# Kernel tuning notes

Hardware: AMD Instinct MI355X
Metric: run time of the kernel (lower is better)

Reference implementation:

```python
import jax, jax.numpy as jnp
import numpy as np

B, C, H, W = 16, 64, 64, 64
HW = H * W            # = dim = 4096
R = 4                 # reduction_ratio
NH = 8                # head_num
EPS = 1e-5


def setup_inputs() -> dict:
    key = jax.random.key(0)
    ks = jax.random.split(key, 8)
    s = 0.02  # weight init scale
    return {
        "x": jax.random.normal(ks[0], (B, C, H, W), jnp.float32),
        "ln1_w": jnp.ones((C,), jnp.float32),
        "ln1_b": jnp.zeros((C,), jnp.float32),
        "ln2_w": jnp.ones((C,), jnp.float32),
        "ln2_b": jnp.zeros((C,), jnp.float32),
        "W_rk": jax.random.normal(ks[1], (C * R, C), jnp.float32) * s,
        "W_rv": jax.random.normal(ks[2], (C * R, C), jnp.float32) * s,
        "W_q": jax.random.normal(ks[3], (HW, HW), jnp.float32) * s,
        "W_k": jax.random.normal(ks[4], (HW // R, HW // R), jnp.float32) * s,
        "W_v": jax.random.normal(ks[5], (HW // R, HW // R), jnp.float32) * s,
        "W_o": jax.random.normal(ks[6], (HW, HW), jnp.float32) * s,
    }


def _ln(x, w, b):
    # LayerNorm over last axis
    mu = jnp.mean(x, axis=-1, keepdims=True)
    var = jnp.mean((x - mu) ** 2, axis=-1, keepdims=True)
    return (x - mu) / jnp.sqrt(var + EPS) * w + b


def reference(x, ln1_w, ln1_b, ln2_w, ln2_b, W_rk, W_rv, W_q, W_k, W_v, W_o):
    b, c, h, w = x.shape
    hw = h * w
    # ln1: LayerNorm2d == per-pixel LayerNorm over channels
    xn = _ln(x.transpose(0, 2, 3, 1), ln1_w, ln1_b)      # [B,H,W,C]
    xf = xn.reshape(b, hw, c)                            # [B,HW,C] (row-major HW)
    # K/V spatial reduction: 'a (cd r) b -> a cd (b r)'
    kv = xf.reshape(b, hw // R, R, c).transpose(0, 1, 3, 2).reshape(b, hw // R, c * R)
    k = _ln(kv @ W_rk, ln2_w, ln2_b)                     # [B,HW/R,C]
    v = _ln(kv @ W_rv, ln2_w, ln2_b)                     # [B,HW/R,C]
    # projections over the SPATIAL axis (dim = HW)
    q = xf.transpose(0, 2, 1) @ W_q                      # [B,C,HW]
    k = k.transpose(0, 2, 1) @ W_k                       # [B,C,HW/R]
    v = v.transpose(0, 2, 1) @ W_v                       # [B,C,HW/R]
    Lq = hw // NH
    Lk = (hw // R) // NH
    # split heads along spatial axis, attend over channel dim C
    qh = q.reshape(b, c, NH, Lq).transpose(0, 2, 3, 1)   # [B,h,Lq,C]
    kh = k.reshape(b, c, NH, Lk).transpose(0, 2, 3, 1)   # [B,h,Lk,C]
    vh = v.reshape(b, c, NH, Lk).transpose(0, 2, 3, 1)   # [B,h,Lk,C]
    scale = float(hw // NH) ** 0.5
    attn = jax.nn.softmax(jnp.einsum('bhqc,bhkc->bhqk', qh, kh) / scale, axis=-1)
    # dropout is identity at inference
    o = jnp.einsum('bhqk,bhkc->bhqc', attn, vh)          # [B,h,Lq,C]
    # concat_head: heads become outer blocks of the spatial axis
    o = o.transpose(0, 3, 1, 2).reshape(b, c, hw)        # [B,C,HW]
    o = o @ W_o                                          # [B,C,HW]
    return o.reshape(b, c, h, w) + x
```

## Files before the change

### kernel.cpp

```cpp
#include <hip/hip_runtime.h>

typedef unsigned short u16;
typedef unsigned int u32;
typedef __attribute__((ext_vector_type(8))) __bf16 bf16x8;
typedef __attribute__((ext_vector_type(4))) float f32x4;
typedef __attribute__((ext_vector_type(4))) unsigned int u32x4;

#define MFMA16(a, b, c) __builtin_amdgcn_mfma_f32_16x16x32_bf16((a), (b), (c), 0, 0, 0)

__device__ __forceinline__ u16 f2bf(float f) {
  unsigned u = __float_as_uint(f);
  u += 0x7FFFu + ((u >> 16) & 1u);
  return (u16)(u >> 16);
}

typedef __attribute__((address_space(1))) const unsigned char gU8;
typedef __attribute__((address_space(3))) unsigned char sU8;
__device__ __forceinline__ void gload16(const void* g, void* l) {
  __builtin_amdgcn_global_load_lds((gU8*)g, (sU8*)l, 16, 0, 0);
}

__device__ __forceinline__ void wt_body(const float* __restrict__ W, u16* __restrict__ Wt,
                                        int K, int N, int bid, float* tile) {
  int ntn = N >> 6;
  int kt = bid / ntn, nt = bid % ntn;
  int t = threadIdx.x;
  const float* src = W + (size_t)kt * 64 * N + (size_t)nt * 64;
  f32x4 r[4];
#pragma unroll
  for (int i = 0; i < 4; ++i) {
    int idx = t + i * 256, row = idx >> 4, c4 = idx & 15;
    r[i] = *(const f32x4*)&src[(size_t)row * N + c4 * 4];
  }
#pragma unroll
  for (int i = 0; i < 4; ++i) {
    int idx = t + i * 256, row = idx >> 4, c4 = idx & 15;
#pragma unroll
    for (int j = 0; j < 4; ++j) tile[row * 65 + c4 * 4 + j] = r[i][j];
  }
  __syncthreads();
  int nn0 = t >> 3, k8 = t & 7;
  float v[2][8];
#pragma unroll
  for (int i = 0; i < 2; ++i)
#pragma unroll
    for (int j = 0; j < 8; ++j) v[i][j] = tile[(k8 * 8 + j) * 65 + nn0 + i * 32];
  u16* dst = Wt + (size_t)nt * 64 * K + (size_t)kt * 64;
#pragma unroll
  for (int i = 0; i < 2; ++i) {
    u32x4 pk;
#pragma unroll
    for (int j = 0; j < 4; ++j)
      pk[j] = (u32)f2bf(v[i][2 * j]) | ((u32)f2bf(v[i][2 * j + 1]) << 16);
    *(u32x4*)&dst[(size_t)(nn0 + i * 32) * K + k8 * 8] = pk;
  }
}

__device__ __forceinline__ void wperm_body(const float* __restrict__ Wrk, const float* __restrict__ Wrv,
                                           u16* __restrict__ Wtk, u16* __restrict__ Wtv, int bid) {
  int idx = bid * 256 + threadIdx.x;
  int cp = idx >> 8, f = idx & 255;
  int k = ((f & 63) << 2) | (f >> 6);
  Wtk[idx] = f2bf(Wrk[k * 64 + cp]);
  Wtv[idx] = f2bf(Wrv[k * 64 + cp]);
}

__device__ __forceinline__ void ln1_body(const float* __restrict__ x, const float* __restrict__ w,
                                         const float* __restrict__ bias, u16* __restrict__ xf_pc,
                                         u16* __restrict__ xfT, int bid, float* tile) {
  int b = bid >> 6, p0 = (bid & 63) << 6;
  int t = threadIdx.x;
  const float* xb = x + (size_t)b * 64 * 4096;
  f32x4 r[4];
#pragma unroll
  for (int i = 0; i < 4; ++i) {
    int idx = t + i * 256, c = idx >> 4, p4 = idx & 15;
    r[i] = *(const f32x4*)&xb[(size_t)c * 4096 + p0 + p4 * 4];
  }
#pragma unroll
  for (int i = 0; i < 4; ++i) {
    int idx = t + i * 256, c = idx >> 4, p4 = idx & 15;
#pragma unroll
    for (int j = 0; j < 4; ++j) tile[c * 65 + p4 * 4 + j] = r[i][j];
  }
  __syncthreads();
  int lane = t & 63, wvx = t >> 6;
  float gw = w[lane], gb = bias[lane];
#pragma unroll
  for (int pp = 0; pp < 16; pp += 2) {
    int p = wvx * 16 + pp;
    float v0 = tile[lane * 65 + p], v1 = tile[lane * 65 + p + 1];
    float s0 = v0, q0 = v0 * v0, s1 = v1, q1 = v1 * v1;
#pragma unroll
    for (int m = 1; m < 64; m <<= 1) {
      s0 += __shfl_xor(s0, m); q0 += __shfl_xor(q0, m);
      s1 += __shfl_xor(s1, m); q1 += __shfl_xor(q1, m);
    }
    float mu0 = s0 * (1.0f / 64.0f), var0 = q0 * (1.0f / 64.0f) - mu0 * mu0;
    float mu1 = s1 * (1.0f / 64.0f), var1 = q1 * (1.0f / 64.0f) - mu1 * mu1;
    tile[lane * 65 + p]     = (v0 - mu0) * rsqrtf(var0 + 1e-5f) * gw + gb;
    tile[lane * 65 + p + 1] = (v1 - mu1) * rsqrtf(var1 + 1e-5f) * gw + gb;
  }
  __syncthreads();
  u16* xfb = xf_pc + (size_t)b * 4096 * 64;
  u16* xtb = xfT + (size_t)b * 64 * 4096;
  int i0 = t >> 3, j8 = t & 7;
  float vc[2][8];
#pragma unroll
  for (int i = 0; i < 2; ++i)
#pragma unroll
    for (int j = 0; j < 8; ++j) vc[i][j] = tile[(j8 * 8 + j) * 65 + i0 + i * 32];
#pragma unroll
  for (int i = 0; i < 2; ++i) {
    u32x4 pk;
#pragma unroll
    for (int j = 0; j < 4; ++j)
      pk[j] = (u32)f2bf(vc[i][2 * j]) | ((u32)f2bf(vc[i][2 * j + 1]) << 16);
    *(u32x4*)&xfb[(size_t)(p0 + i0 + i * 32) * 64 + j8 * 8] = pk;
  }
  float vr[2][8];
#pragma unroll
  for (int i = 0; i < 2; ++i)
#pragma unroll
    for (int j = 0; j < 8; ++j) vr[i][j] = tile[(i0 + i * 32) * 65 + j8 * 8 + j];
#pragma unroll
  for (int i = 0; i < 2; ++i) {
    u32x4 pk;
#pragma unroll
    for (int j = 0; j < 4; ++j)
      pk[j] = (u32)f2bf(vr[i][2 * j]) | ((u32)f2bf(vr[i][2 * j + 1]) << 16);
    *(u32x4*)&xtb[(size_t)(i0 + i * 32) * 4096 + p0 + j8 * 8] = pk;
  }
}

__global__ __launch_bounds__(256) void prep_kernel(
    const float* __restrict__ W_q, u16* __restrict__ Wt_q,
    const float* __restrict__ W_o, u16* __restrict__ Wt_o,
    const float* __restrict__ W_k, u16* __restrict__ Wt_k,
    const float* __restrict__ W_v, u16* __restrict__ Wt_v,
    const float* __restrict__ W_rk, const float* __restrict__ W_rv,
    u16* __restrict__ Wt_rk, u16* __restrict__ Wt_rv,
    const float* __restrict__ x, const float* __restrict__ ln1w, const float* __restrict__ ln1b,
    u16* __restrict__ xf_pc, u16* __restrict__ xfT) {
  __shared__ float tile[64 * 65];
  int bid = blockIdx.x;
  if (bid < 4096)       wt_body(W_q, Wt_q, 4096, 4096, bid, tile);
  else if (bid < 8192)  wt_body(W_o, Wt_o, 4096, 4096, bid - 4096, tile);
  else if (bid < 8448)  wt_body(W_k, Wt_k, 1024, 1024, bid - 8192, tile);
  else if (bid < 8704)  wt_body(W_v, Wt_v, 1024, 1024, bid - 8448, tile);
  else if (bid < 8768)  wperm_body(W_rk, W_rv, Wt_rk, Wt_rv, bid - 8704);
  else                  ln1_body(x, ln1w, ln1b, xf_pc, xfT, bid - 8768, tile);
}

__global__ __launch_bounds__(256) void kv_kernel(const u16* __restrict__ xf_pc,
                                                 const u16* __restrict__ Wtk, const u16* __restrict__ Wtv,
                                                 const float* __restrict__ ln2w, const float* __restrict__ ln2b,
                                                 u16* __restrict__ kT, u16* __restrict__ vT) {
  __shared__ __align__(16) u16 As[64 * 264];
  __shared__ __align__(16) u16 Bk[64 * 264];
  __shared__ __align__(16) u16 Bv[64 * 264];
  u16* Tk = As;
  u16* Tv = As + 64 * 72;
  int b = blockIdx.x >> 4, s0 = (blockIdx.x & 15) << 6;
  int t = threadIdx.x;
  const u16* Asrc = xf_pc + (size_t)b * 4096 * 64 + (size_t)s0 * 256;
#pragma unroll
  for (int i = 0; i < 8; ++i) {
    int id = t + i * 256, row = id >> 5, c16 = id & 31;
    *(u32x4*)&As[row * 264 + c16 * 8] = *(const u32x4*)&Asrc[(size_t)row * 256 + c16 * 8];
    *(u32x4*)&Bk[row * 264 + c16 * 8] = *(const u32x4*)&Wtk[(size_t)row * 256 + c16 * 8];
    *(u32x4*)&Bv[row * 264 + c16 * 8] = *(const u32x4*)&Wtv[(size_t)row * 256 + c16 * 8];
  }
  __syncthreads();
  int lane = t & 63, wv = t >> 6, lo = lane & 15, hi = lane >> 4;
  f32x4 acck[4] = {}, accv[4] = {};
  int arow = (wv * 16 + lo) * 264 + hi * 8;
#pragma unroll
  for (int kk = 0; kk < 8; ++kk) {
    bf16x8 a = *(const bf16x8*)&As[arow + kk * 32];
#pragma unroll
    for (int nf = 0; nf < 4; ++nf) {
      bf16x8 bk = *(const bf16x8*)&Bk[(nf * 16 + lo) * 264 + kk * 32 + hi * 8];
      bf16x8 bv = *(const bf16x8*)&Bv[(nf * 16 + lo) * 264 + kk * 32 + hi * 8];
      acck[nf] = MFMA16(a, bk, acck[nf]);
      accv[nf] = MFMA16(a, bv, accv[nf]);
    }
  }
  __syncthreads();
  float w2[4], b2[4];
#pragma unroll
  for (int nf = 0; nf < 4; ++nf) { w2[nf] = ln2w[nf * 16 + lo]; b2[nf] = ln2b[nf * 16 + lo]; }
#pragma unroll
  for (int r = 0; r < 4; ++r) {
    float sk = 0.f, sk2 = 0.f, sv = 0.f, sv2 = 0.f;
#pragma unroll
    for (int nf = 0; nf < 4; ++nf) {
      float a = acck[nf][r], c = accv[nf][r];
      sk += a; sk2 += a * a; sv += c; sv2 += c * c;
    }
#pragma unroll
    for (int m = 1; m < 16; m <<= 1) {
      sk += __shfl_xor(sk, m); sk2 += __shfl_xor(sk2, m);
      sv += __shfl_xor(sv, m); sv2 += __shfl_xor(sv2, m);
    }
    float mk = sk * (1.f / 64.f), vk = sk2 * (1.f / 64.f) - mk * mk, rk = rsqrtf(vk + 1e-5f);
    float mv = sv * (1.f / 64.f), vv = sv2 * (1.f / 64.f) - mv * mv, rv = rsqrtf(vv + 1e-5f);
    int srow = wv * 16 + hi * 4 + r;
#pragma unroll
    for (int nf = 0; nf < 4; ++nf) {
      Tk[(nf * 16 + lo) * 72 + srow] = f2bf((acck[nf][r] - mk) * rk * w2[nf] + b2[nf]);
      Tv[(nf * 16 + lo) * 72 + srow] = f2bf((accv[nf][r] - mv) * rv * w2[nf] + b2[nf]);
    }
  }
  __syncthreads();
  u16* kdst = kT + (size_t)b * 64 * 1024 + s0;
  u16* vdst = vT + (size_t)b * 64 * 1024 + s0;
#pragma unroll
  for (int i = 0; i < 16; ++i) {
    int idx = t + i * 256, cp = idx >> 6, s = idx & 63;
    kdst[(size_t)cp * 1024 + s] = Tk[cp * 72 + s];
    vdst[(size_t)cp * 1024 + s] = Tv[cp * 72 + s];
  }
}

__device__ __forceinline__ void stage32(const u16* Ab, const u16* Bb, int K, int kt,
                                        u16* As, u16* Bs, int wv, int lane) {
#pragma unroll
  for (int i = 0; i < 2; ++i) {
    int cb = wv * 2 + i;
    int c = cb * 64 + lane;
    int row = c >> 2, s = c & 3;
    int scol = (s ^ (row & 3)) << 3;
    gload16(Ab + (size_t)row * K + kt * 32 + scol, As + cb * 512);
    gload16(Bb + (size_t)row * K + kt * 32 + scol, Bs + cb * 512);
  }
}

__device__ __forceinline__ void compute32(const u16* As, const u16* Bs, f32x4 acc[4][4],
                                          int wm, int wn, int lo, int hi) {
  int slot = (hi ^ (lo & 3)) << 3;
  bf16x8 a[4], bb[4];
#pragma unroll
  for (int i = 0; i < 4; ++i) {
    a[i]  = *(const bf16x8*)&As[(wm + i * 16 + lo) * 32 + slot];
    bb[i] = *(const bf16x8*)&Bs[(wn + i * 16 + lo) * 32 + slot];
  }
#pragma unroll
  for (int mi = 0; mi < 4; ++mi)
#pragma unroll
    for (int ni = 0; ni < 4; ++ni)
      acc[mi][ni] = MFMA16(a[mi], bb[ni], acc[mi][ni]);
}

template <int EPI>
__device__ void gemm_body(const u16* __restrict__ A, const u16* __restrict__ Bm,
                          u16* __restrict__ Cc, int N, int K, int chunkStride,
                          int mt, int nt, int koff, int nk, u16* lds) {
  int t = threadIdx.x, lane = t & 63, wv = t >> 6;
  int wm = (wv >> 1) * 64, wn = (wv & 1) * 64;
  int lo = lane & 15, hi = lane >> 4;
  f32x4 acc[4][4] = {};
  const u16* Ab = A + (size_t)mt * 128 * K + koff;
  const u16* Bb = Bm + (size_t)nt * 128 * K + koff;
  u16* bufs[3] = {lds, lds + 8192, lds + 16384};
  stage32(Ab, Bb, K, 0, bufs[0], bufs[0] + 4096, wv, lane);
  stage32(Ab, Bb, K, 1, bufs[1], bufs[1] + 4096, wv, lane);
  for (int kt = 0; kt < nk; ++kt) {
    if (kt + 1 < nk) asm volatile("s_waitcnt vmcnt(4)" ::: "memory");
    else             asm volatile("s_waitcnt vmcnt(0)" ::: "memory");
    __builtin_amdgcn_s_barrier();
    __builtin_amdgcn_sched_barrier(0);
    if (kt + 2 < nk) {
      u16* nb = bufs[(kt + 2) % 3];
      stage32(Ab, Bb, K, kt + 2, nb, nb + 4096, wv, lane);
    }
    u16* cb = bufs[kt % 3];
    compute32(cb, cb + 4096, acc, wm, wn, lo, hi);
  }
#pragma unroll
  for (int mi = 0; mi < 4; ++mi)
#pragma unroll
    for (int ni = 0; ni < 4; ++ni)
#pragma unroll
      for (int r = 0; r < 4; ++r) {
        int m = mt * 128 + wm + mi * 16 + hi * 4 + r;
        int n = nt * 128 + wn + ni * 16 + lo;
        float v = acc[mi][ni][r];
        if constexpr (EPI == 0) {
          Cc[(size_t)m * N + n] = f2bf(v);
        } else {
          Cc[(size_t)(n >> 6) * chunkStride + (size_t)m * 64 + (n & 63)] = f2bf(v);
        }
      }
}

__global__ __launch_bounds__(256, 3) void qkv_kernel(
    const u16* __restrict__ Wt_q, const u16* __restrict__ xfT, u16* __restrict__ q_t,
    const u16* __restrict__ Wt_k, const u16* __restrict__ k_lnT, u16* __restrict__ kproj,
    const u16* __restrict__ v_lnT, const u16* __restrict__ Wt_v, u16* __restrict__ vproj) {
  __shared__ __align__(16) u16 lds[24576];
  int bid = blockIdx.x;
  if (bid < 1024) {
    int log = (bid & 7) * 128 + (bid >> 3);
    int kh = log >> 8, tile = log & 255, mt = tile >> 3, nt = tile & 7;
    gemm_body<1>(Wt_q, xfT, q_t + (size_t)kh * 4194304, 1024, 4096, 4096 * 64,
                 mt, nt, kh * 1024, 32, lds);
  } else if (bid < 1088) {
    int id = bid - 1024;
    gemm_body<1>(Wt_k, k_lnT, kproj, 1024, 1024, 1024 * 64, id >> 3, id & 7, 0, 32, lds);
  } else {
    int id = bid - 1088;
    gemm_body<0>(v_lnT, Wt_v, vproj, 1024, 1024, 0, id >> 3, id & 7, 0, 32, lds);
  }
}

__global__ __launch_bounds__(256, 3) void ogemm_kernel(const u16* __restrict__ o2,
                                                       const u16* __restrict__ Wt_o,
                                                       u16* __restrict__ o_part) {
  __shared__ __align__(16) u16 lds[24576];
  int bid = blockIdx.x;
  int log = (bid & 7) * 64 + (bid >> 3);
  int kh = log >> 8, tile = log & 255, mt = tile >> 5, nt = tile & 31;
  gemm_body<0>(o2, Wt_o, o_part + (size_t)kh * 4194304, 4096, 4096, 0,
               mt, nt, kh * 2048, 64, lds);
}

__global__ __launch_bounds__(256) void oreduce_kernel(const float* __restrict__ x,
                                                      const u16* __restrict__ p0,
                                                      const u16* __restrict__ p1,
                                                      float* __restrict__ out) {
  size_t base = ((size_t)blockIdx.x * 256 + threadIdx.x) * 8;
  u32x4 a = *(const u32x4*)&p0[base];
  u32x4 b = *(const u32x4*)&p1[base];
  f32x4 x0 = *(const f32x4*)&x[base];
  f32x4 x1 = *(const f32x4*)&x[base + 4];
  float r[8];
#pragma unroll
  for (int j = 0; j < 4; ++j) {
    r[2 * j]     = __uint_as_float(a[j] << 16) + __uint_as_float(b[j] << 16);
    r[2 * j + 1] = __uint_as_float(a[j] & 0xFFFF0000u) + __uint_as_float(b[j] & 0xFFFF0000u);
  }
  f32x4 o0, o1;
#pragma unroll
  for (int j = 0; j < 4; ++j) { o0[j] = r[j] + x0[j]; o1[j] = r[4 + j] + x1[j]; }
  *(f32x4*)&out[base] = o0;
  *(f32x4*)&out[base + 4] = o1;
}

__global__ __launch_bounds__(256) void attn_kernel(const u16* __restrict__ qp, const u16* __restrict__ kp,
                                                   const u16* __restrict__ vp, u16* __restrict__ o2) {
  __shared__ __align__(16) u16 Qs[128 * 72];
  __shared__ __align__(16) u16 Ks[128 * 72];
  __shared__ __align__(16) u16 Vs[64 * 136];
  __shared__ __align__(16) u16 Ps[128 * 136];
  int qt = blockIdx.x & 3, h = (blockIdx.x >> 2) & 7, b = blockIdx.x >> 5;
  int t = threadIdx.x, lane = t & 63, wv = t >> 6;
  int lo = lane & 15, hi = lane >> 4;
  const u16* qsrc = qp + (size_t)b * 262144 + (size_t)(h * 512 + qt * 128) * 64;
  const u16* ksrc = kp + (size_t)b * 1024 * 64 + (size_t)(h * 128) * 64;
  const u16* vsrc = vp + (size_t)b * 64 * 1024 + h * 128;
#pragma unroll
  for (int i = 0; i < 4; ++i) {
    int id = t + i * 256, row = id >> 3, c8 = id & 7;
    size_t goff = (size_t)row * 64 + c8 * 8;
    float f[8] = {0.f, 0.f, 0.f, 0.f, 0.f, 0.f, 0.f, 0.f};
#pragma unroll
    for (int kh = 0; kh < 4; ++kh) {
      u32x4 pk = *(const u32x4*)&qsrc[(size_t)kh * 4194304 + goff];
#pragma unroll
      for (int j = 0; j < 4; ++j) {
        f[2 * j]     += __uint_as_float(pk[j] << 16);
        f[2 * j + 1] += __uint_as_float(pk[j] & 0xFFFF0000u);
      }
    }
    u32x4 pko;
#pragma unroll
    for (int j = 0; j < 4; ++j) pko[j] = (u32)f2bf(f[2 * j]) | ((u32)f2bf(f[2 * j + 1]) << 16);
    *(u32x4*)&Qs[row * 72 + c8 * 8] = pko;
  }
#pragma unroll
  for (int i = 0; i < 4; ++i) {
    int id = t + i * 256;
    int row = id >> 3, c16 = id & 7;
    *(u32x4*)&Ks[row * 72 + c16 * 8] = *(const u32x4*)&ksrc[(size_t)row * 64 + c16 * 8];
    int vrow = id >> 4, v16 = id & 15;
    *(u32x4*)&Vs[vrow * 136 + v16 * 8] = *(const u32x4*)&vsrc[(size_t)vrow * 1024 + v16 * 8];
  }
  __syncthreads();
  f32x4 s[2][8] = {};
#pragma unroll
  for (int kk = 0; kk < 2; ++kk) {
    bf16x8 a0 = *(const bf16x8*)&Qs[(wv * 32 + lo) * 72 + kk * 32 + hi * 8];
    bf16x8 a1 = *(const bf16x8*)&Qs[(wv * 32 + 16 + lo) * 72 + kk * 32 + hi * 8];
#pragma unroll
    for (int ni = 0; ni < 8; ++ni) {
      bf16x8 bb = *(const bf16x8*)&Ks[(ni * 16 + lo) * 72 + kk * 32 + hi * 8];
      s[0][ni] = MFMA16(a0, bb, s[0][ni]);
      s[1][ni] = MFMA16(a1, bb, s[1][ni]);
    }
  }
  const float inv_scale = 0.044194173824159216f;
#pragma unroll
  for (int mi = 0; mi < 2; ++mi)
#pragma unroll
    for (int ni = 0; ni < 8; ++ni) s[mi][ni] *= inv_scale;
#pragma unroll
  for (int mi = 0; mi < 2; ++mi) {
#pragma unroll
    for (int r = 0; r < 4; ++r) {
      float mx = -1e30f;
#pragma unroll
      for (int ni = 0; ni < 8; ++ni) mx = fmaxf(mx, s[mi][ni][r]);
#pragma unroll
      for (int m = 1; m < 16; m <<= 1) mx = fmaxf(mx, __shfl_xor(mx, m));
      float p[8], sum = 0.f;
#pragma unroll
      for (int ni = 0; ni < 8; ++ni) { p[ni] = __expf(s[mi][ni][r] - mx); sum += p[ni]; }
#pragma unroll
      for (int m = 1; m < 16; m <<= 1) sum += __shfl_xor(sum, m);
      float rs = 1.0f / sum;
      int row = wv * 32 + mi * 16 + hi * 4 + r;
#pragma unroll
      for (int ni = 0; ni < 8; ++ni) Ps[row * 136 + ni * 16 + lo] = f2bf(p[ni] * rs);
    }
  }
  __syncthreads();
  f32x4 o[4][2] = {};
#pragma unroll
  for (int kk = 0; kk < 4; ++kk) {
    bf16x8 b0 = *(const bf16x8*)&Ps[(wv * 32 + lo) * 136 + kk * 32 + hi * 8];
    bf16x8 b1 = *(const bf16x8*)&Ps[(wv * 32 + 16 + lo) * 136 + kk * 32 + hi * 8];
#pragma unroll
    for (int mi = 0; mi < 4; ++mi) {
      bf16x8 a = *(const bf16x8*)&Vs[(mi * 16 + lo) * 136 + kk * 32 + hi * 8];
      o[mi][0] = MFMA16(a, b0, o[mi][0]);
      o[mi][1] = MFMA16(a, b1, o[mi][1]);
    }
  }
  u16* od = o2 + (size_t)b * 64 * 4096 + h * 512 + qt * 128;
#pragma unroll
  for (int mi = 0; mi < 4; ++mi)
#pragma unroll
    for (int ni = 0; ni < 2; ++ni)
#pragma unroll
      for (int r = 0; r < 4; ++r) {
        int c = mi * 16 + hi * 4 + r;
        int lq = wv * 32 + ni * 16 + lo;
        od[(size_t)c * 4096 + lq] = f2bf(o[mi][ni][r]);
      }
}

extern "C" void kernel_launch(void* const* d_in, const int* in_sizes, int n_in,
                              void* d_out, int out_size, void* d_ws, size_t ws_size,
                              hipStream_t stream) {
  (void)in_sizes; (void)n_in; (void)out_size; (void)ws_size;
  const float* x    = (const float*)d_in[0];
  const float* ln1w = (const float*)d_in[1];
  const float* ln1b = (const float*)d_in[2];
  const float* ln2w = (const float*)d_in[3];
  const float* ln2b = (const float*)d_in[4];
  const float* W_rk = (const float*)d_in[5];
  const float* W_rv = (const float*)d_in[6];
  const float* W_q  = (const float*)d_in[7];
  const float* W_k  = (const float*)d_in[8];
  const float* W_v  = (const float*)d_in[9];
  const float* W_o  = (const float*)d_in[10];

  char* ws = (char*)d_ws;
  size_t off = 0;
  auto alloc = [&](size_t bytes) { char* p = ws + off; off += bytes; return p; };
  u16* Wt_q  = (u16*)alloc(4096ull * 4096 * 2);
  u16* Wt_o  = (u16*)alloc(4096ull * 4096 * 2);
  u16* Wt_k  = (u16*)alloc(1024ull * 1024 * 2);
  u16* Wt_v  = (u16*)alloc(1024ull * 1024 * 2);
  u16* Wt_rk = (u16*)alloc(64ull * 256 * 2);
  u16* Wt_rv = (u16*)alloc(64ull * 256 * 2);
  u16* xf_pc = (u16*)alloc(16ull * 4096 * 64 * 2);
  u16* xfT   = (u16*)alloc(16ull * 64 * 4096 * 2);
  u16* k_lnT = (u16*)alloc(16ull * 64 * 1024 * 2);
  u16* v_lnT = (u16*)alloc(16ull * 64 * 1024 * 2);
  u16* q_t   = (u16*)alloc(4ull * 16 * 4096 * 64 * 2);
  u16* kproj = (u16*)alloc(16ull * 1024 * 64 * 2);
  u16* vproj = (u16*)alloc(16ull * 64 * 1024 * 2);
  u16* o2     = xfT;
  u16* o_part = Wt_q;

  prep_kernel<<<9792, 256, 0, stream>>>(W_q, Wt_q, W_o, Wt_o, W_k, Wt_k, W_v, Wt_v,
                                        W_rk, W_rv, Wt_rk, Wt_rv, x, ln1w, ln1b, xf_pc, xfT);
  kv_kernel<<<256, 256, 0, stream>>>(xf_pc, Wt_rk, Wt_rv, ln2w, ln2b, k_lnT, v_lnT);
  qkv_kernel<<<1152, 256, 0, stream>>>(Wt_q, xfT, q_t, Wt_k, k_lnT, kproj, v_lnT, Wt_v, vproj);
  attn_kernel<<<512, 256, 0, stream>>>(q_t, kproj, vproj, o2);
  ogemm_kernel<<<512, 256, 0, stream>>>(o2, Wt_o, o_part);
  oreduce_kernel<<<2048, 256, 0, stream>>>(x, o_part, o_part + 4194304, (float*)d_out);
}
```

Measured before the change: 212.9 us.

## Fuse fp32 weight transpose and bf16 conversion into GEMM staging

Drops the separate prep pass that transposed W_q, W_o, W_k and W_v into bf16 workspace copies. The GEMMs now load fp32 weight tiles straight into registers, convert them to bf16 and write them into swizzled LDS, while the activation operand still uses async global-to-LDS loads. This removes a large read/write round trip of the weight matrices, at the cost of more global bytes per GEMM (fp32 instead of bf16), extra register pressure, and conversion work inside the pipelined main loop.

Measured after the change: 329.3 us. 54.7% more time.

```diff
diff --git a/kernel.cpp b/kernel.cpp
--- a/kernel.cpp
+++ b/kernel.cpp
@@ -18,42 +18,6 @@
 typedef __attribute__((address_space(3))) unsigned char sU8;
 __device__ __forceinline__ void gload16(const void* g, void* l) {
   __builtin_amdgcn_global_load_lds((gU8*)g, (sU8*)l, 16, 0, 0);
-}
-
-__device__ __forceinline__ void wt_body(const float* __restrict__ W, u16* __restrict__ Wt,
-                                        int K, int N, int bid, float* tile) {
-  int ntn = N >> 6;
-  int kt = bid / ntn, nt = bid % ntn;
-  int t = threadIdx.x;
-  const float* src = W + (size_t)kt * 64 * N + (size_t)nt * 64;
-  f32x4 r[4];
-#pragma unroll
-  for (int i = 0; i < 4; ++i) {
-    int idx = t + i * 256, row = idx >> 4, c4 = idx & 15;
-    r[i] = *(const f32x4*)&src[(size_t)row * N + c4 * 4];
-  }
-#pragma unroll
-  for (int i = 0; i < 4; ++i) {
-    int idx = t + i * 256, row = idx >> 4, c4 = idx & 15;
-#pragma unroll
-    for (int j = 0; j < 4; ++j) tile[row * 65 + c4 * 4 + j] = r[i][j];
-  }
-  __syncthreads();
-  int nn0 = t >> 3, k8 = t & 7;
-  float v[2][8];
-#pragma unroll
-  for (int i = 0; i < 2; ++i)
-#pragma unroll
-    for (int j = 0; j < 8; ++j) v[i][j] = tile[(k8 * 8 + j) * 65 + nn0 + i * 32];
-  u16* dst = Wt + (size_t)nt * 64 * K + (size_t)kt * 64;
-#pragma unroll
-  for (int i = 0; i < 2; ++i) {
-    u32x4 pk;
-#pragma unroll
-    for (int j = 0; j < 4; ++j)
-      pk[j] = (u32)f2bf(v[i][2 * j]) | ((u32)f2bf(v[i][2 * j + 1]) << 16);
-    *(u32x4*)&dst[(size_t)(nn0 + i * 32) * K + k8 * 8] = pk;
-  }
 }
 
 __device__ __forceinline__ void wperm_body(const float* __restrict__ Wrk, const float* __restrict__ Wrv,
@@ -134,22 +98,14 @@
 }
 
 __global__ __launch_bounds__(256) void prep_kernel(
-    const float* __restrict__ W_q, u16* __restrict__ Wt_q,
-    const float* __restrict__ W_o, u16* __restrict__ Wt_o,
-    const float* __restrict__ W_k, u16* __restrict__ Wt_k,
-    const float* __restrict__ W_v, u16* __restrict__ Wt_v,
     const float* __restrict__ W_rk, const float* __restrict__ W_rv,
     u16* __restrict__ Wt_rk, u16* __restrict__ Wt_rv,
     const float* __restrict__ x, const float* __restrict__ ln1w, const float* __restrict__ ln1b,
     u16* __restrict__ xf_pc, u16* __restrict__ xfT) {
   __shared__ float tile[64 * 65];
   int bid = blockIdx.x;
-  if (bid < 4096)       wt_body(W_q, Wt_q, 4096, 4096, bid, tile);
-  else if (bid < 8192)  wt_body(W_o, Wt_o, 4096, 4096, bid - 4096, tile);
-  else if (bid < 8448)  wt_body(W_k, Wt_k, 1024, 1024, bid - 8192, tile);
-  else if (bid < 8704)  wt_body(W_v, Wt_v, 1024, 1024, bid - 8448, tile);
-  else if (bid < 8768)  wperm_body(W_rk, W_rv, Wt_rk, Wt_rv, bid - 8704);
-  else                  ln1_body(x, ln1w, ln1b, xf_pc, xfT, bid - 8768, tile);
+  if (bid < 64) wperm_body(W_rk, W_rv, Wt_rk, Wt_rv, bid);
+  else          ln1_body(x, ln1w, ln1b, xf_pc, xfT, bid - 64, tile);
 }
 
 __global__ __launch_bounds__(256) void kv_kernel(const u16* __restrict__ xf_pc,
@@ -223,22 +179,46 @@
   }
 }
 
-__device__ __forceinline__ void stage32(const u16* Ab, const u16* Bb, int K, int kt,
-                                        u16* As, u16* Bs, int wv, int lane) {
+
+__device__ __forceinline__ void wload(const float* __restrict__ Wsrc, int Nw, int kbase, int wbase,
+                                      int t, f32x4 rr[4]) {
+  int r = t >> 4, j0 = (t & 15) * 4;
+  const float* p0 = Wsrc + (size_t)(kbase + 2 * r) * Nw + wbase + j0;
+  rr[0] = *(const f32x4*)p0;
+  rr[1] = *(const f32x4*)(p0 + Nw);
+  rr[2] = *(const f32x4*)(p0 + 64);
+  rr[3] = *(const f32x4*)(p0 + Nw + 64);
+}
+
+__device__ __forceinline__ void wstore(const f32x4 rr[4], int t, u16* As) {
+  int r = t >> 4, j0 = (t & 15) * 4;
+  int o = (2 * r) & 7;
+  int c = r >> 2;
+#pragma unroll
+  for (int i = 0; i < 2; ++i)
+#pragma unroll
+    for (int jj = 0; jj < 4; ++jj) {
+      int j = j0 + i * 64 + jj;
+      int s = c ^ ((j >> 2) & 3);
+      u32 pk = (u32)f2bf(rr[2 * i][jj]) | ((u32)f2bf(rr[2 * i + 1][jj]) << 16);
+      *(u32*)&As[j * 32 + s * 8 + o] = pk;
+    }
+}
+
+__device__ __forceinline__ void stageG(const u16* Gb, int K, int kt, u16* Bs, int wv, int lane) {
 #pragma unroll
   for (int i = 0; i < 2; ++i) {
     int cb = wv * 2 + i;
     int c = cb * 64 + lane;
     int row = c >> 2, s = c & 3;
-    int scol = (s ^ (row & 3)) << 3;
-    gload16(Ab + (size_t)row * K + kt * 32 + scol, As + cb * 512);
-    gload16(Bb + (size_t)row * K + kt * 32 + scol, Bs + cb * 512);
+    int scol = (s ^ ((row >> 2) & 3)) << 3;
+    gload16(Gb + (size_t)row * K + kt * 32 + scol, Bs + cb * 512);
   }
 }
 
 __device__ __forceinline__ void compute32(const u16* As, const u16* Bs, f32x4 acc[4][4],
                                           int wm, int wn, int lo, int hi) {
-  int slot = (hi ^ (lo & 3)) << 3;
+  int slot = (hi ^ ((lo >> 2) & 3)) << 3;
   bf16x8 a[4], bb[4];
 #pragma unroll
   for (int i = 0; i < 4; ++i) {
@@ -252,30 +232,64 @@
       acc[mi][ni] = MFMA16(a[mi], bb[ni], acc[mi][ni]);
 }
 
-template <int EPI>
-__device__ void gemm_body(const u16* __restrict__ A, const u16* __restrict__ Bm,
-                          u16* __restrict__ Cc, int N, int K, int chunkStride,
-                          int mt, int nt, int koff, int nk, u16* lds) {
+template <int EPI, int SIDE>
+__device__ void gemm_bodyW(const float* __restrict__ Wsrc, int Nw,
+                           const u16* __restrict__ Gm,
+                           u16* __restrict__ Cc, int N, int K, int chunkStride,
+                           int mt, int nt, int koff, int nk, u16* lds) {
   int t = threadIdx.x, lane = t & 63, wv = t >> 6;
   int wm = (wv >> 1) * 64, wn = (wv & 1) * 64;
   int lo = lane & 15, hi = lane >> 4;
   f32x4 acc[4][4] = {};
-  const u16* Ab = A + (size_t)mt * 128 * K + koff;
-  const u16* Bb = Bm + (size_t)nt * 128 * K + koff;
-  u16* bufs[3] = {lds, lds + 8192, lds + 16384};
-  stage32(Ab, Bb, K, 0, bufs[0], bufs[0] + 4096, wv, lane);
-  stage32(Ab, Bb, K, 1, bufs[1], bufs[1] + 4096, wv, lane);
-  for (int kt = 0; kt < nk; ++kt) {
-    if (kt + 1 < nk) asm volatile("s_waitcnt vmcnt(4)" ::: "memory");
-    else             asm volatile("s_waitcnt vmcnt(0)" ::: "memory");
+  int wbase = (SIDE == 0 ? mt : nt) * 128;
+  const u16* Gb = Gm + (size_t)(SIDE == 0 ? nt : mt) * 128 * K + koff;
+  u16* SW[3]; u16* SG[3];
+#pragma unroll
+  for (int b = 0; b < 3; ++b) {
+    u16* base = lds + b * 8192;
+    SW[b] = base;
+    SG[b] = base + 4096;
+  }
+  f32x4 rA[4], rB[4];
+  wload(Wsrc, Nw, koff, wbase, t, rA);
+  stageG(Gb, K, 0, SG[0], wv, lane);
+  wload(Wsrc, Nw, koff + 32, wbase, t, rB);
+  stageG(Gb, K, 1, SG[1], wv, lane);
+  wstore(rA, t, SW[0]);
+  for (int kt = 0; kt < nk; kt += 2) {
+    asm volatile("s_waitcnt vmcnt(2)" ::: "memory");
+    wstore(rB, t, SW[(kt + 1) % 3]);
+    asm volatile("s_waitcnt lgkmcnt(0)" ::: "memory");
     __builtin_amdgcn_s_barrier();
     __builtin_amdgcn_sched_barrier(0);
     if (kt + 2 < nk) {
-      u16* nb = bufs[(kt + 2) % 3];
-      stage32(Ab, Bb, K, kt + 2, nb, nb + 4096, wv, lane);
-    }
-    u16* cb = bufs[kt % 3];
-    compute32(cb, cb + 4096, acc, wm, wn, lo, hi);
+      wload(Wsrc, Nw, koff + (kt + 2) * 32, wbase, t, rA);
+      stageG(Gb, K, kt + 2, SG[(kt + 2) % 3], wv, lane);
+    }
+    {
+      u16* A_ = SIDE == 0 ? SW[kt % 3] : SG[kt % 3];
+      u16* B_ = SIDE == 0 ? SG[kt % 3] : SW[kt % 3];
+      compute32(A_, B_, acc, wm, wn, lo, hi);
+    }
+    int k1 = kt + 1;
+    if (k1 + 1 < nk) {
+      asm volatile("s_waitcnt vmcnt(2)" ::: "memory");
+      wstore(rA, t, SW[(k1 + 1) % 3]);
+    } else {
+      asm volatile("s_waitcnt vmcnt(0)" ::: "memory");
+    }
+    asm volatile("s_waitcnt lgkmcnt(0)" ::: "memory");
+    __builtin_amdgcn_s_barrier();
+    __builtin_amdgcn_sched_barrier(0);
+    if (k1 + 2 < nk) {
+      wload(Wsrc, Nw, koff + (k1 + 2) * 32, wbase, t, rB);
+      stageG(Gb, K, k1 + 2, SG[(k1 + 2) % 3], wv, lane);
+    }
+    {
+      u16* A_ = SIDE == 0 ? SW[k1 % 3] : SG[k1 % 3];
+      u16* B_ = SIDE == 0 ? SG[k1 % 3] : SW[k1 % 3];
+      compute32(A_, B_, acc, wm, wn, lo, hi);
+    }
   }
 #pragma unroll
   for (int mi = 0; mi < 4; ++mi)
@@ -295,34 +309,34 @@
 }
 
 __global__ __launch_bounds__(256, 3) void qkv_kernel(
-    const u16* __restrict__ Wt_q, const u16* __restrict__ xfT, u16* __restrict__ q_t,
-    const u16* __restrict__ Wt_k, const u16* __restrict__ k_lnT, u16* __restrict__ kproj,
-    const u16* __restrict__ v_lnT, const u16* __restrict__ Wt_v, u16* __restrict__ vproj) {
+    const float* __restrict__ W_q, const u16* __restrict__ xfT, u16* __restrict__ q_t,
+    const float* __restrict__ W_k, const u16* __restrict__ k_lnT, u16* __restrict__ kproj,
+    const u16* __restrict__ v_lnT, const float* __restrict__ W_v, u16* __restrict__ vproj) {
   __shared__ __align__(16) u16 lds[24576];
   int bid = blockIdx.x;
   if (bid < 1024) {
     int log = (bid & 7) * 128 + (bid >> 3);
     int kh = log >> 8, tile = log & 255, mt = tile >> 3, nt = tile & 7;
-    gemm_body<1>(Wt_q, xfT, q_t + (size_t)kh * 4194304, 1024, 4096, 4096 * 64,
-                 mt, nt, kh * 1024, 32, lds);
+    gemm_bodyW<1, 0>(W_q, 4096, xfT, q_t + (size_t)kh * 4194304, 1024, 4096, 4096 * 64,
+                     mt, nt, kh * 1024, 32, lds);
   } else if (bid < 1088) {
     int id = bid - 1024;
-    gemm_body<1>(Wt_k, k_lnT, kproj, 1024, 1024, 1024 * 64, id >> 3, id & 7, 0, 32, lds);
+    gemm_bodyW<1, 0>(W_k, 1024, k_lnT, kproj, 1024, 1024, 1024 * 64, id >> 3, id & 7, 0, 32, lds);
   } else {
     int id = bid - 1088;
-    gemm_body<0>(v_lnT, Wt_v, vproj, 1024, 1024, 0, id >> 3, id & 7, 0, 32, lds);
+    gemm_bodyW<0, 1>(W_v, 1024, v_lnT, vproj, 1024, 1024, 0, id >> 3, id & 7, 0, 32, lds);
   }
 }
 
 __global__ __launch_bounds__(256, 3) void ogemm_kernel(const u16* __restrict__ o2,
-                                                       const u16* __restrict__ Wt_o,
+                                                       const float* __restrict__ W_o,
                                                        u16* __restrict__ o_part) {
   __shared__ __align__(16) u16 lds[24576];
   int bid = blockIdx.x;
   int log = (bid & 7) * 64 + (bid >> 3);
   int kh = log >> 8, tile = log & 255, mt = tile >> 5, nt = tile & 31;
-  gemm_body<0>(o2, Wt_o, o_part + (size_t)kh * 4194304, 4096, 4096, 0,
-               mt, nt, kh * 2048, 64, lds);
+  gemm_bodyW<0, 1>(W_o, 4096, o2, o_part + (size_t)kh * 4194304, 4096, 4096, 0,
+                   mt, nt, kh * 2048, 64, lds);
 }
 
 __global__ __launch_bounds__(256) void oreduce_kernel(const float* __restrict__ x,
@@ -469,27 +483,22 @@
   char* ws = (char*)d_ws;
   size_t off = 0;
   auto alloc = [&](size_t bytes) { char* p = ws + off; off += bytes; return p; };
-  u16* Wt_q  = (u16*)alloc(4096ull * 4096 * 2);
-  u16* Wt_o  = (u16*)alloc(4096ull * 4096 * 2);
-  u16* Wt_k  = (u16*)alloc(1024ull * 1024 * 2);
-  u16* Wt_v  = (u16*)alloc(1024ull * 1024 * 2);
-  u16* Wt_rk = (u16*)alloc(64ull * 256 * 2);
-  u16* Wt_rv = (u16*)alloc(64ull * 256 * 2);
-  u16* xf_pc = (u16*)alloc(16ull * 4096 * 64 * 2);
-  u16* xfT   = (u16*)alloc(16ull * 64 * 4096 * 2);
-  u16* k_lnT = (u16*)alloc(16ull * 64 * 1024 * 2);
-  u16* v_lnT = (u16*)alloc(16ull * 64 * 1024 * 2);
-  u16* q_t   = (u16*)alloc(4ull * 16 * 4096 * 64 * 2);
-  u16* kproj = (u16*)alloc(16ull * 1024 * 64 * 2);
-  u16* vproj = (u16*)alloc(16ull * 64 * 1024 * 2);
+  u16* o_part = (u16*)alloc(2ull * 16 * 4096 * 64 * 2);
+  u16* Wt_rk  = (u16*)alloc(64ull * 256 * 2);
+  u16* Wt_rv  = (u16*)alloc(64ull * 256 * 2);
+  u16* xf_pc  = (u16*)alloc(16ull * 4096 * 64 * 2);
+  u16* xfT    = (u16*)alloc(16ull * 64 * 4096 * 2);
+  u16* k_lnT  = (u16*)alloc(16ull * 64 * 1024 * 2);
+  u16* v_lnT  = (u16*)alloc(16ull * 64 * 1024 * 2);
+  u16* q_t    = (u16*)alloc(4ull * 16 * 4096 * 64 * 2);
+  u16* kproj  = (u16*)alloc(16ull * 1024 * 64 * 2);
+  u16* vproj  = (u16*)alloc(16ull * 64 * 1024 * 2);
   u16* o2     = xfT;
-  u16* o_part = Wt_q;
-
-  prep_kernel<<<9792, 256, 0, stream>>>(W_q, Wt_q, W_o, Wt_o, W_k, Wt_k, W_v, Wt_v,
-                                        W_rk, W_rv, Wt_rk, Wt_rv, x, ln1w, ln1b, xf_pc, xfT);
+
+  prep_kernel<<<1088, 256, 0, stream>>>(W_rk, W_rv, Wt_rk, Wt_rv, x, ln1w, ln1b, xf_pc, xfT);
   kv_kernel<<<256, 256, 0, stream>>>(xf_pc, Wt_rk, Wt_rv, ln2w, ln2b, k_lnT, v_lnT);
-  qkv_kernel<<<1152, 256, 0, stream>>>(Wt_q, xfT, q_t, Wt_k, k_lnT, kproj, v_lnT, Wt_v, vproj);
+  qkv_kernel<<<1152, 256, 0, stream>>>(W_q, xfT, q_t, W_k, k_lnT, kproj, v_lnT, W_v, vproj);
   attn_kernel<<<512, 256, 0, stream>>>(q_t, kproj, vproj, o2);
-  ogemm_kernel<<<512, 256, 0, stream>>>(o2, Wt_o, o_part);
+  ogemm_kernel<<<512, 256, 0, stream>>>(o2, W_o, o_part);
   oreduce_kernel<<<2048, 256, 0, stream>>>(x, o_part, o_part + 4194304, (float*)d_out);
 }
```
